# Kernel optimization log

Hardware: AMD Instinct MI355X
Metric: run time of the kernel (lower is better)

## Reference

```python
import jax, jax.numpy as jnp
import numpy as np

NUM_HEADS = 16
DIM = 1024
B, L = 2, 2048
NEG = -10000000000.0


def setup_inputs() -> dict:
    key = jax.random.key(0)
    ks = jax.random.split(key, 8)
    queries = jax.random.normal(ks[0], (B, L, DIM), dtype=jnp.float32)
    keys = jax.random.normal(ks[1], (B, L, DIM), dtype=jnp.float32)
    values = jax.random.normal(ks[2], (B, L, DIM), dtype=jnp.float32)
    mask = jax.random.uniform(ks[3], (B, L, L)) < 0.1
    s = 1.0 / np.sqrt(DIM)
    Wq = jax.random.uniform(ks[4], (DIM, DIM), minval=-s, maxval=s, dtype=jnp.float32)
    Wk = jax.random.uniform(ks[5], (DIM, DIM), minval=-s, maxval=s, dtype=jnp.float32)
    Wv = jax.random.uniform(ks[6], (DIM, DIM), minval=-s, maxval=s, dtype=jnp.float32)
    Wo = jax.random.uniform(ks[7], (DIM, DIM), minval=-s, maxval=s, dtype=jnp.float32)
    return {"queries": queries, "keys": keys, "values": values, "mask": mask,
            "Wq": Wq, "Wk": Wk, "Wv": Wv, "Wo": Wo}


def reference(queries, keys, values, mask, Wq, Wk, Wv, Wo):
    b, l, d = queries.shape
    h = NUM_HEADS
    dk = d // h
    # torch Linear(bias=False): y = x @ W.T ; then view(b, l, dk, h) -> head axis LAST
    qs = (queries @ Wq.T).reshape(b, l, dk, h)
    ks = (keys @ Wk.T).reshape(b, l, dk, h)
    vs = (values @ Wv.T).reshape(b, l, dk, h)
    # routing is None in the live code path
    w = jnp.einsum('bidh,bodh->bioh', qs, ks) / jnp.sqrt(jnp.asarray(dk, jnp.float32))
    w = jnp.where(mask[..., None], NEG, w)          # masked_fill where mask True
    w = jax.nn.softmax(w, axis=-2)                   # softmax over key axis 'o'
    mha = jnp.einsum('bioh,bodh->bidh', w, vs).reshape(b, l, d)
    # dropout is identity in eval mode
    return mha @ Wo.T
```

## Files before the change

kernel.cpp:

```cpp
#include <hip/hip_runtime.h>
#include <hip/hip_bf16.h>
#include <cstdint>
#include <cstddef>

typedef unsigned short ushort_t;
typedef __attribute__((ext_vector_type(8))) short short8;
typedef __attribute__((ext_vector_type(8))) unsigned short ushort8;
typedef __attribute__((ext_vector_type(4))) unsigned short ushort4v;
typedef __attribute__((ext_vector_type(4))) float f32x4;
typedef __attribute__((ext_vector_type(2))) unsigned long long ull2;

#define LPAD 72

__device__ __forceinline__ unsigned short f2bf(float f) {
    unsigned int x = __float_as_uint(f);
    unsigned int r = x + 0x7fffu + ((x >> 16) & 1u);
    return (unsigned short)(r >> 16);
}

__device__ __forceinline__ void async16(const ushort_t* g, ushort_t* l) {
    __builtin_amdgcn_global_load_lds(
        (const __attribute__((address_space(1))) unsigned int*)g,
        (__attribute__((address_space(3))) unsigned int*)l,
        16, 0, 0);
}

__global__ __launch_bounds__(256) void cvt(const float* __restrict__ q,
                                           const float* __restrict__ k,
                                           const float* __restrict__ v,
                                           const float* __restrict__ Wq,
                                           const float* __restrict__ Wk,
                                           const float* __restrict__ Wv,
                                           ushort_t* __restrict__ qb,
                                           ushort_t* __restrict__ kb,
                                           ushort_t* __restrict__ vb,
                                           ushort_t* __restrict__ Wqb,
                                           ushort_t* __restrict__ Wkb,
                                           ushort_t* __restrict__ Wvb) {
    const int z = blockIdx.y;
    const float* X = (z == 0) ? q : (z == 1) ? k : v;
    const float* W = (z == 0) ? Wq : (z == 1) ? Wk : Wv;
    ushort_t* Xo = (z == 0) ? qb : (z == 1) ? kb : vb;
    ushort_t* Wo2 = (z == 0) ? Wqb : (z == 1) ? Wkb : Wvb;
    const size_t idx = (((size_t)blockIdx.x << 8) + threadIdx.x) << 3;
    const float* src; ushort_t* dst; float sc = 1.0f;
    if (idx < 4194304) { src = X + idx; dst = Xo + idx; if (z == 0) sc = 0.125f; }
    else               { src = W + (idx - 4194304); dst = Wo2 + (idx - 4194304); }
    f32x4 a0 = *(const f32x4*)src, a1 = *(const f32x4*)(src + 4);
    ushort8 o;
    #pragma unroll
    for (int j = 0; j < 4; j++) { o[j] = f2bf(a0[j] * sc); o[j + 4] = f2bf(a1[j] * sc); }
    *(ushort8*)dst = o;
}

__global__ __launch_bounds__(256) void maskbits_kernel(const int* __restrict__ mask,
                                                       unsigned long long* __restrict__ Mbits) {
    const int row  = blockIdx.x;
    const int w    = threadIdx.x >> 6;
    const int lane = threadIdx.x & 63;
    const int* mrow = mask + (size_t)row * 2048;
    #pragma unroll
    for (int it = 0; it < 8; it++) {
        const int o = (it << 8) + (w << 6) + lane;
        const unsigned long long bb = __ballot(mrow[o] != 0);
        if (lane == 0) Mbits[(size_t)((it << 2) + w) * 4096 + row] = bb;
    }
}

__global__ __launch_bounds__(256) void woswz(const float* __restrict__ W,
                                             ushort_t* __restrict__ WoH) {
    __shared__ float row[1024 + 64];
    const int j = blockIdx.x, t = threadIdx.x;
    f32x4 v = *(const f32x4*)(W + (size_t)j * 1024 + (t << 2));
    #pragma unroll
    for (int s = 0; s < 4; s++) { const int c = (t << 2) + s; row[c + (c >> 4)] = v[s]; }
    __syncthreads();
    #pragma unroll
    for (int s = 0; s < 4; s++) {
        const int k = t + (s << 8);
        const int col = ((k & 63) << 4) + (k >> 6);
        WoH[(size_t)j * 1024 + k] = f2bf(row[col + (col >> 4)]);
    }
}

__global__ __launch_bounds__(256) void gemm_proj(const ushort_t* __restrict__ qb,
                                                 const ushort_t* __restrict__ kb,
                                                 const ushort_t* __restrict__ vb,
                                                 const ushort_t* __restrict__ Wqb,
                                                 const ushort_t* __restrict__ Wkb,
                                                 const ushort_t* __restrict__ Wvb,
                                                 ushort_t* __restrict__ Qh,
                                                 ushort_t* __restrict__ Kh,
                                                 ushort_t* __restrict__ VhT) {
    __shared__ ushort_t Xs[512 * 8];
    __shared__ ushort_t Ws[512 * 8];

    const int lid  = blockIdx.x;
    const int nIdx = lid / 96;
    const int rem  = lid % 96;
    const int z    = rem >> 5;
    const int mIdx = rem & 31;
    const int n0   = nIdx << 7;
    const int m0   = mIdx << 7;

    const ushort_t* Xb = (z == 0) ? qb : (z == 1) ? kb : vb;
    const ushort_t* Wb = (z == 0) ? Wqb : (z == 1) ? Wkb : Wvb;

    const int tid  = threadIdx.x;
    const int w    = tid >> 6;
    const int lane = tid & 63;
    const int lm   = lane & 15;
    const int quad = lane >> 4;
    const int wm   = w & 1;
    const int wn   = w >> 1;

    f32x4 acc[4][4];
    #pragma unroll
    for (int i = 0; i < 4; i++)
        #pragma unroll
        for (int j = 0; j < 4; j++) acc[i][j] = (f32x4){0.f, 0.f, 0.f, 0.f};

    for (int k0 = 0; k0 < 1024; k0 += 32) {
        __syncthreads();
        #pragma unroll
        for (int i = 0; i < 2; i++) {
            const int L   = (((w << 1) + i) << 6) + lane;
            const int c4  = L >> 7, row = L & 127;
            const int lb  = (((w << 1) + i) << 6) << 3;
            async16(Xb + (size_t)(m0 + row) * 1024 + k0 + (c4 << 3), &Xs[lb]);
            async16(Wb + (size_t)(n0 + row) * 1024 + k0 + (c4 << 3), &Ws[lb]);
        }
        __syncthreads();
        short8 af[4], bf4[4];
        #pragma unroll
        for (int mf = 0; mf < 4; mf++)
            af[mf] = *(const short8*)&Xs[((quad << 7) + (wm << 6) + (mf << 4) + lm) << 3];
        #pragma unroll
        for (int nf = 0; nf < 4; nf++)
            bf4[nf] = *(const short8*)&Ws[((quad << 7) + (wn << 6) + (nf << 4) + lm) << 3];
        #pragma unroll
        for (int mf = 0; mf < 4; mf++)
            #pragma unroll
            for (int nf = 0; nf < 4; nf++)
                acc[mf][nf] = __builtin_amdgcn_mfma_f32_16x16x32_bf16(af[mf], bf4[nf], acc[mf][nf], 0, 0, 0);
    }

    const int bb    = m0 >> 11;
    const int l0    = m0 & 2047;
    const int dbase = (n0 >> 4) + (wn << 2);
    if (z != 2) {
        ushort_t* OUT = (z == 0) ? Qh : Kh;
        #pragma unroll
        for (int mf = 0; mf < 4; mf++)
            #pragma unroll
            for (int r = 0; r < 4; r++) {
                const int row = (wm << 6) + (mf << 4) + (quad << 2) + r;
                ushort4v o = { f2bf(acc[mf][0][r]), f2bf(acc[mf][1][r]),
                               f2bf(acc[mf][2][r]), f2bf(acc[mf][3][r]) };
                *(ushort4v*)(OUT + ((size_t)((bb << 4) + lm) * 2048 + l0 + row) * 64 + dbase) = o;
            }
    } else {
        #pragma unroll
        for (int mf = 0; mf < 4; mf++)
            #pragma unroll
            for (int nf = 0; nf < 4; nf++) {
                const int lbase = l0 + (wm << 6) + (mf << 4) + (quad << 2);
                ushort4v o = { f2bf(acc[mf][nf][0]), f2bf(acc[mf][nf][1]),
                               f2bf(acc[mf][nf][2]), f2bf(acc[mf][nf][3]) };
                *(ushort4v*)(VhT + ((size_t)((bb << 4) + lm) * 64 + dbase + nf) * 2048 + lbase) = o;
            }
    }
}

__global__ __launch_bounds__(256) void gemm_out(const ushort_t* __restrict__ mhaH,
                                                const ushort_t* __restrict__ WoH,
                                                float* __restrict__ C) {
    __shared__ ushort_t Xs[256 * 8];
    __shared__ ushort_t Ws[256 * 8];
    const int tid  = threadIdx.x;
    const int m0   = blockIdx.y << 6;
    const int n0   = blockIdx.x << 6;
    const int w    = tid >> 6;
    const int lane = tid & 63;
    const int lm   = lane & 15;
    const int quad = lane >> 4;
    const int ab   = m0 >> 11;
    const int al0  = m0 & 2047;

    f32x4 acc[4] = {{0.f,0.f,0.f,0.f},{0.f,0.f,0.f,0.f},{0.f,0.f,0.f,0.f},{0.f,0.f,0.f,0.f}};

    for (int k0 = 0; k0 < 1024; k0 += 32) {
        const int h  = k0 >> 6;
        const int d0 = k0 & 63;
        __syncthreads();
        async16(mhaH + (((size_t)(ab * 16 + h)) * 2048 + al0 + lane) * 64 + d0 + (w << 3),
                &Xs[(w << 6) << 3]);
        async16(WoH + (size_t)(n0 + lane) * 1024 + k0 + (w << 3),
                &Ws[(w << 6) << 3]);
        __syncthreads();
        short8 af = *(const short8*)&Xs[((quad << 6) + (w << 4) + lm) << 3];
        #pragma unroll
        for (int c = 0; c < 4; c++) {
            short8 bf = *(const short8*)&Ws[((quad << 6) + (c << 4) + lm) << 3];
            acc[c] = __builtin_amdgcn_mfma_f32_16x16x32_bf16(af, bf, acc[c], 0, 0, 0);
        }
    }
    #pragma unroll
    for (int c = 0; c < 4; c++) {
        #pragma unroll
        for (int r = 0; r < 4; r++) {
            const int row = m0 + (w << 4) + (quad << 2) + r;
            const int col = n0 + (c << 4) + lm;
            C[(size_t)row * 1024 + col] = acc[c][r];
        }
    }
}

__global__ __launch_bounds__(256, 2) void flash_attn(const ushort_t* __restrict__ Qh,
                                                     const ushort_t* __restrict__ Kh,
                                                     const ushort_t* __restrict__ VhT,
                                                     const unsigned long long* __restrict__ Mbits,
                                                     ushort_t* __restrict__ mhaH) {
    __shared__ ushort_t Ks[64 * LPAD];
    __shared__ ushort_t Vt[64 * LPAD];
    __shared__ ushort_t Pw[4][16 * LPAD];

    const int tid  = threadIdx.x;
    const int w    = tid >> 6;
    const int lane = tid & 63;
    const int lm   = lane & 15;
    const int quad = lane >> 4;
    const int bh   = blockIdx.y;
    const int b    = bh >> 4;
    const int q0   = blockIdx.x << 7;

    const ushort_t* Qb  = Qh  + ((size_t)bh << 17);
    const ushort_t* Kb  = Kh  + ((size_t)bh << 17);
    const ushort_t* Vtb = VhT + ((size_t)bh << 17);

    short8 aq[2][2];
    #pragma unroll
    for (int g = 0; g < 2; g++) {
        const ushort_t* qp = Qb + (size_t)(q0 + (w << 5) + (g << 4) + lm) * 64 + (quad << 3);
        aq[g][0] = *(const short8*)qp;
        aq[g][1] = *(const short8*)(qp + 32);
    }

    float l_part[2][4] = {{0.f,0.f,0.f,0.f},{0.f,0.f,0.f,0.f}};
    f32x4 o_acc[2][4] = {{{0.f,0.f,0.f,0.f},{0.f,0.f,0.f,0.f},{0.f,0.f,0.f,0.f},{0.f,0.f,0.f,0.f}},
                         {{0.f,0.f,0.f,0.f},{0.f,0.f,0.f,0.f},{0.f,0.f,0.f,0.f},{0.f,0.f,0.f,0.f}}};

    const int chunk0  = tid << 1;
    const int rowbase = (b << 11) + q0 + (w << 5);

    for (int kt0 = 0; kt0 < 2048; kt0 += 64) {
        __syncthreads();
        #pragma unroll
        for (int cc = 0; cc < 2; cc++) {
            const int chunk = chunk0 + cc;
            const int rr = chunk >> 3;
            const int rc = (chunk & 7) << 3;
            *(ushort8*)&Ks[rr * LPAD + rc] =
                *(const ushort8*)(Kb + (size_t)(kt0 + rr) * 64 + rc);
            *(ushort8*)&Vt[rr * LPAD + rc] =
                *(const ushort8*)(Vtb + (size_t)rr * 2048 + kt0 + rc);
        }
        __syncthreads();

        short8 bk[4][2], bv[4][2];
        #pragma unroll
        for (int c = 0; c < 4; c++) {
            bk[c][0] = *(const short8*)&Ks[((c << 4) + lm) * LPAD + (quad << 3)];
            bk[c][1] = *(const short8*)&Ks[((c << 4) + lm) * LPAD + 32 + (quad << 3)];
            bv[c][0] = *(const short8*)&Vt[((c << 4) + lm) * LPAD + (quad << 3)];
            bv[c][1] = *(const short8*)&Vt[((c << 4) + lm) * LPAD + 32 + (quad << 3)];
        }

        const unsigned long long* Mt = Mbits + (size_t)(kt0 >> 6) * 4096 + rowbase;

        #pragma unroll
        for (int g = 0; g < 2; g++) {
            f32x4 s[4];
            #pragma unroll
            for (int c = 0; c < 4; c++) {
                f32x4 zz = {0.f, 0.f, 0.f, 0.f};
                zz = __builtin_amdgcn_mfma_f32_16x16x32_bf16(aq[g][0], bk[c][0], zz, 0, 0, 0);
                zz = __builtin_amdgcn_mfma_f32_16x16x32_bf16(aq[g][1], bk[c][1], zz, 0, 0, 0);
                s[c] = zz;
            }
            unsigned long long mb[4];
            {
                const unsigned long long* mp = Mt + (g << 4) + (quad << 2);
                ull2 t0 = *(const ull2*)mp;
                ull2 t1 = *(const ull2*)(mp + 2);
                mb[0] = t0[0]; mb[1] = t0[1]; mb[2] = t1[0]; mb[3] = t1[1];
            }
            #pragma unroll
            for (int r = 0; r < 4; r++) {
                const unsigned lo = (unsigned)mb[r];
                const unsigned hi = (unsigned)(mb[r] >> 32);
                float lsum = 0.f;
                #pragma unroll
                for (int c = 0; c < 4; c++) {
                    const unsigned word = (c & 2) ? hi : lo;
                    const unsigned bit = (word >> (((c & 1) << 4) + lm)) & 1u;
                    const float p = bit ? 0.f : __expf(s[c][r]);
                    s[c][r] = p;
                    lsum += p;
                }
                l_part[g][r] += lsum;
            }
            #pragma unroll
            for (int c = 0; c < 4; c++)
                #pragma unroll
                for (int r = 0; r < 4; r++)
                    Pw[w][((quad << 2) + r) * LPAD + (c << 4) + lm] = f2bf(s[c][r]);

            short8 ap0 = *(const short8*)&Pw[w][lm * LPAD + (quad << 3)];
            short8 ap1 = *(const short8*)&Pw[w][lm * LPAD + 32 + (quad << 3)];
            #pragma unroll
            for (int cd = 0; cd < 4; cd++) {
                o_acc[g][cd] = __builtin_amdgcn_mfma_f32_16x16x32_bf16(ap0, bv[cd][0], o_acc[g][cd], 0, 0, 0);
                o_acc[g][cd] = __builtin_amdgcn_mfma_f32_16x16x32_bf16(ap1, bv[cd][1], o_acc[g][cd], 0, 0, 0);
            }
        }
    }

    #pragma unroll
    for (int g = 0; g < 2; g++) {
        #pragma unroll
        for (int r = 0; r < 4; r++) {
            float l = l_part[g][r];
            l += __shfl_xor(l, 1, 64);
            l += __shfl_xor(l, 2, 64);
            l += __shfl_xor(l, 4, 64);
            l += __shfl_xor(l, 8, 64);
            const float inv_l = 1.0f / l;
            const int i = q0 + (w << 5) + (g << 4) + (quad << 2) + r;
            ushort_t* orow = mhaH + (((size_t)bh * 2048 + i) << 6);
            #pragma unroll
            for (int cd = 0; cd < 4; cd++)
                orow[(cd << 4) + lm] = f2bf(o_acc[g][cd][r] * inv_l);
        }
    }
}

extern "C" void kernel_launch(void* const* d_in, const int* in_sizes, int n_in,
                              void* d_out, int out_size, void* d_ws, size_t ws_size,
                              hipStream_t stream) {
    const float* q    = (const float*)d_in[0];
    const float* k    = (const float*)d_in[1];
    const float* v    = (const float*)d_in[2];
    const int*   mask = (const int*)d_in[3];
    const float* Wq   = (const float*)d_in[4];
    const float* Wk   = (const float*)d_in[5];
    const float* Wv   = (const float*)d_in[6];
    const float* Wo   = (const float*)d_in[7];
    float* out = (float*)d_out;

    ushort_t* qb   = (ushort_t*)d_ws;
    ushort_t* kb   = qb  + 4194304;
    ushort_t* vb   = kb  + 4194304;
    ushort_t* Wqb  = vb  + 4194304;
    ushort_t* Wkb  = Wqb + 1048576;
    ushort_t* Wvb  = Wkb + 1048576;
    ushort_t* Qh   = Wvb + 1048576;
    ushort_t* Kh   = Qh  + 4194304;
    ushort_t* VhT  = Kh  + 4194304;
    ushort_t* mhaH = qb;
    ushort_t* WoH  = kb;
    unsigned long long* Mbits = (unsigned long long*)(kb + 1048576);

    dim3 gb(256);
    cvt<<<dim3(2560, 3), gb, 0, stream>>>(q, k, v, Wq, Wk, Wv, qb, kb, vb, Wqb, Wkb, Wvb);
    gemm_proj<<<dim3(768), gb, 0, stream>>>(qb, kb, vb, Wqb, Wkb, Wvb, Qh, Kh, VhT);
    maskbits_kernel<<<dim3(4096), gb, 0, stream>>>(mask, Mbits);
    woswz<<<dim3(1024), gb, 0, stream>>>(Wo, WoH);
    flash_attn<<<dim3(16, 32), gb, 0, stream>>>(Qh, Kh, VhT, Mbits, mhaH);
    gemm_out<<<dim3(16, 64), gb, 0, stream>>>(mhaH, WoH, out);
}
```

Measured before the change: 326.9 us.

## Retile projection per head and load K/V fragments directly in attention

The projection GEMM now assigns each block one head (64 output columns gathered with stride 16) instead of 128 contiguous columns. This doubles the grid and changes the Q/K/V write pattern to per-head rows. The attention kernel drops its shared-memory K/V staging and the two barriers per tile, reading MFMA fragments straight from global memory. It also swaps the QK^T operand order so each lane owns one query row, which simplifies mask-bit extraction to one 64-bit load and lets the P tile be packed as 4-wide stores. The risks are uncoalesced, redundant global K/V reads across waves and a strided weight gather in the projection.

After: 379.1 us. 1.16x slower.

```diff
diff --git a/kernel.cpp b/kernel.cpp
--- a/kernel.cpp
+++ b/kernel.cpp
@@ -8,7 +8,6 @@
 typedef __attribute__((ext_vector_type(8))) unsigned short ushort8;
 typedef __attribute__((ext_vector_type(4))) unsigned short ushort4v;
 typedef __attribute__((ext_vector_type(4))) float f32x4;
-typedef __attribute__((ext_vector_type(2))) unsigned long long ull2;
 
 #define LPAD 72
 
@@ -93,14 +92,13 @@
                                                  ushort_t* __restrict__ Kh,
                                                  ushort_t* __restrict__ VhT) {
     __shared__ ushort_t Xs[512 * 8];
-    __shared__ ushort_t Ws[512 * 8];
+    __shared__ ushort_t Ws[256 * 8];
 
     const int lid  = blockIdx.x;
-    const int nIdx = lid / 96;
-    const int rem  = lid % 96;
-    const int z    = rem >> 5;
-    const int mIdx = rem & 31;
-    const int n0   = nIdx << 7;
+    const int z    = lid % 3;
+    const int rem  = lid / 3;
+    const int head = rem & 15;
+    const int mIdx = rem >> 4;
     const int m0   = mIdx << 7;
 
     const ushort_t* Xb = (z == 0) ? qb : (z == 1) ? kb : vb;
@@ -114,11 +112,11 @@
     const int wm   = w & 1;
     const int wn   = w >> 1;
 
-    f32x4 acc[4][4];
+    f32x4 acc[4][2];
     #pragma unroll
     for (int i = 0; i < 4; i++)
         #pragma unroll
-        for (int j = 0; j < 4; j++) acc[i][j] = (f32x4){0.f, 0.f, 0.f, 0.f};
+        for (int j = 0; j < 2; j++) acc[i][j] = (f32x4){0.f, 0.f, 0.f, 0.f};
 
     for (int k0 = 0; k0 < 1024; k0 += 32) {
         __syncthreads();
@@ -126,48 +124,54 @@
         for (int i = 0; i < 2; i++) {
             const int L   = (((w << 1) + i) << 6) + lane;
             const int c4  = L >> 7, row = L & 127;
-            const int lb  = (((w << 1) + i) << 6) << 3;
-            async16(Xb + (size_t)(m0 + row) * 1024 + k0 + (c4 << 3), &Xs[lb]);
-            async16(Wb + (size_t)(n0 + row) * 1024 + k0 + (c4 << 3), &Ws[lb]);
+            async16(Xb + (size_t)(m0 + row) * 1024 + k0 + (c4 << 3),
+                    &Xs[((((w << 1) + i) << 6) << 3)]);
+        }
+        {
+            const int j = head + (lane << 4);
+            async16(Wb + (size_t)j * 1024 + k0 + (w << 3), &Ws[((w << 6) << 3)]);
         }
         __syncthreads();
-        short8 af[4], bf4[4];
+        short8 af[4], bf2[2];
         #pragma unroll
         for (int mf = 0; mf < 4; mf++)
             af[mf] = *(const short8*)&Xs[((quad << 7) + (wm << 6) + (mf << 4) + lm) << 3];
         #pragma unroll
-        for (int nf = 0; nf < 4; nf++)
-            bf4[nf] = *(const short8*)&Ws[((quad << 7) + (wn << 6) + (nf << 4) + lm) << 3];
+        for (int nf = 0; nf < 2; nf++)
+            bf2[nf] = *(const short8*)&Ws[((quad << 6) + (wn << 5) + (nf << 4) + lm) << 3];
         #pragma unroll
         for (int mf = 0; mf < 4; mf++)
             #pragma unroll
-            for (int nf = 0; nf < 4; nf++)
-                acc[mf][nf] = __builtin_amdgcn_mfma_f32_16x16x32_bf16(af[mf], bf4[nf], acc[mf][nf], 0, 0, 0);
-    }
-
-    const int bb    = m0 >> 11;
-    const int l0    = m0 & 2047;
-    const int dbase = (n0 >> 4) + (wn << 2);
+            for (int nf = 0; nf < 2; nf++)
+                acc[mf][nf] = __builtin_amdgcn_mfma_f32_16x16x32_bf16(af[mf], bf2[nf], acc[mf][nf], 0, 0, 0);
+    }
+
+    const int bb = m0 >> 11;
+    const int l0 = m0 & 2047;
+    const size_t bh = (size_t)((bb << 4) + head);
     if (z != 2) {
         ushort_t* OUT = (z == 0) ? Qh : Kh;
         #pragma unroll
         for (int mf = 0; mf < 4; mf++)
             #pragma unroll
-            for (int r = 0; r < 4; r++) {
-                const int row = (wm << 6) + (mf << 4) + (quad << 2) + r;
-                ushort4v o = { f2bf(acc[mf][0][r]), f2bf(acc[mf][1][r]),
-                               f2bf(acc[mf][2][r]), f2bf(acc[mf][3][r]) };
-                *(ushort4v*)(OUT + ((size_t)((bb << 4) + lm) * 2048 + l0 + row) * 64 + dbase) = o;
+            for (int nf = 0; nf < 2; nf++) {
+                const int d = (wn << 5) + (nf << 4) + lm;
+                #pragma unroll
+                for (int r = 0; r < 4; r++) {
+                    const int l = l0 + (wm << 6) + (mf << 4) + (quad << 2) + r;
+                    OUT[((bh * 2048 + l) << 6) + d] = f2bf(acc[mf][nf][r]);
+                }
             }
     } else {
         #pragma unroll
         for (int mf = 0; mf < 4; mf++)
             #pragma unroll
-            for (int nf = 0; nf < 4; nf++) {
-                const int lbase = l0 + (wm << 6) + (mf << 4) + (quad << 2);
+            for (int nf = 0; nf < 2; nf++) {
+                const int d = (wn << 5) + (nf << 4) + lm;
+                const int l = l0 + (wm << 6) + (mf << 4) + (quad << 2);
                 ushort4v o = { f2bf(acc[mf][nf][0]), f2bf(acc[mf][nf][1]),
                                f2bf(acc[mf][nf][2]), f2bf(acc[mf][nf][3]) };
-                *(ushort4v*)(VhT + ((size_t)((bb << 4) + lm) * 64 + dbase + nf) * 2048 + lbase) = o;
+                *(ushort4v*)(VhT + ((bh << 6) + d) * 2048 + l) = o;
             }
     }
 }
@@ -221,8 +225,6 @@
                                                      const ushort_t* __restrict__ VhT,
                                                      const unsigned long long* __restrict__ Mbits,
                                                      ushort_t* __restrict__ mhaH) {
-    __shared__ ushort_t Ks[64 * LPAD];
-    __shared__ ushort_t Vt[64 * LPAD];
     __shared__ ushort_t Pw[4][16 * LPAD];
 
     const int tid  = threadIdx.x;
@@ -238,45 +240,32 @@
     const ushort_t* Kb  = Kh  + ((size_t)bh << 17);
     const ushort_t* Vtb = VhT + ((size_t)bh << 17);
 
-    short8 aq[2][2];
+    short8 bq[2][2];
     #pragma unroll
     for (int g = 0; g < 2; g++) {
         const ushort_t* qp = Qb + (size_t)(q0 + (w << 5) + (g << 4) + lm) * 64 + (quad << 3);
-        aq[g][0] = *(const short8*)qp;
-        aq[g][1] = *(const short8*)(qp + 32);
-    }
-
-    float l_part[2][4] = {{0.f,0.f,0.f,0.f},{0.f,0.f,0.f,0.f}};
+        bq[g][0] = *(const short8*)qp;
+        bq[g][1] = *(const short8*)(qp + 32);
+    }
+
+    float l_part[2] = {0.f, 0.f};
     f32x4 o_acc[2][4] = {{{0.f,0.f,0.f,0.f},{0.f,0.f,0.f,0.f},{0.f,0.f,0.f,0.f},{0.f,0.f,0.f,0.f}},
                          {{0.f,0.f,0.f,0.f},{0.f,0.f,0.f,0.f},{0.f,0.f,0.f,0.f},{0.f,0.f,0.f,0.f}}};
 
-    const int chunk0  = tid << 1;
-    const int rowbase = (b << 11) + q0 + (w << 5);
+    const int rowq = (b << 11) + q0 + (w << 5);
 
     for (int kt0 = 0; kt0 < 2048; kt0 += 64) {
-        __syncthreads();
-        #pragma unroll
-        for (int cc = 0; cc < 2; cc++) {
-            const int chunk = chunk0 + cc;
-            const int rr = chunk >> 3;
-            const int rc = (chunk & 7) << 3;
-            *(ushort8*)&Ks[rr * LPAD + rc] =
-                *(const ushort8*)(Kb + (size_t)(kt0 + rr) * 64 + rc);
-            *(ushort8*)&Vt[rr * LPAD + rc] =
-                *(const ushort8*)(Vtb + (size_t)rr * 2048 + kt0 + rc);
-        }
-        __syncthreads();
-
-        short8 bk[4][2], bv[4][2];
+        short8 ak[4][2], bv[4][2];
         #pragma unroll
         for (int c = 0; c < 4; c++) {
-            bk[c][0] = *(const short8*)&Ks[((c << 4) + lm) * LPAD + (quad << 3)];
-            bk[c][1] = *(const short8*)&Ks[((c << 4) + lm) * LPAD + 32 + (quad << 3)];
-            bv[c][0] = *(const short8*)&Vt[((c << 4) + lm) * LPAD + (quad << 3)];
-            bv[c][1] = *(const short8*)&Vt[((c << 4) + lm) * LPAD + 32 + (quad << 3)];
-        }
-
-        const unsigned long long* Mt = Mbits + (size_t)(kt0 >> 6) * 4096 + rowbase;
+            const ushort_t* kp = Kb + (size_t)(kt0 + (c << 4) + lm) * 64 + (quad << 3);
+            ak[c][0] = *(const short8*)kp;
+            ak[c][1] = *(const short8*)(kp + 32);
+            const ushort_t* vp = Vtb + (size_t)((c << 4) + lm) * 2048 + kt0 + (quad << 3);
+            bv[c][0] = *(const short8*)vp;
+            bv[c][1] = *(const short8*)(vp + 32);
+        }
+        const unsigned long long* Mt = Mbits + ((size_t)(kt0 >> 6) << 12) + rowq;
 
         #pragma unroll
         for (int g = 0; g < 2; g++) {
@@ -284,38 +273,28 @@
             #pragma unroll
             for (int c = 0; c < 4; c++) {
                 f32x4 zz = {0.f, 0.f, 0.f, 0.f};
-                zz = __builtin_amdgcn_mfma_f32_16x16x32_bf16(aq[g][0], bk[c][0], zz, 0, 0, 0);
-                zz = __builtin_amdgcn_mfma_f32_16x16x32_bf16(aq[g][1], bk[c][1], zz, 0, 0, 0);
+                zz = __builtin_amdgcn_mfma_f32_16x16x32_bf16(ak[c][0], bq[g][0], zz, 0, 0, 0);
+                zz = __builtin_amdgcn_mfma_f32_16x16x32_bf16(ak[c][1], bq[g][1], zz, 0, 0, 0);
                 s[c] = zz;
             }
-            unsigned long long mb[4];
-            {
-                const unsigned long long* mp = Mt + (g << 4) + (quad << 2);
-                ull2 t0 = *(const ull2*)mp;
-                ull2 t1 = *(const ull2*)(mp + 2);
-                mb[0] = t0[0]; mb[1] = t0[1]; mb[2] = t1[0]; mb[3] = t1[1];
-            }
-            #pragma unroll
-            for (int r = 0; r < 4; r++) {
-                const unsigned lo = (unsigned)mb[r];
-                const unsigned hi = (unsigned)(mb[r] >> 32);
-                float lsum = 0.f;
+            const unsigned long long M = Mt[(g << 4) + lm];
+            float lsum = 0.f;
+            #pragma unroll
+            for (int c = 0; c < 4; c++) {
                 #pragma unroll
-                for (int c = 0; c < 4; c++) {
-                    const unsigned word = (c & 2) ? hi : lo;
-                    const unsigned bit = (word >> (((c & 1) << 4) + lm)) & 1u;
+                for (int r = 0; r < 4; r++) {
+                    const unsigned bit = (unsigned)(M >> ((c << 4) + (quad << 2) + r)) & 1u;
                     const float p = bit ? 0.f : __expf(s[c][r]);
                     s[c][r] = p;
                     lsum += p;
                 }
-                l_part[g][r] += lsum;
-            }
-            #pragma unroll
-            for (int c = 0; c < 4; c++)
-                #pragma unroll
-                for (int r = 0; r < 4; r++)
-                    Pw[w][((quad << 2) + r) * LPAD + (c << 4) + lm] = f2bf(s[c][r]);
-
+            }
+            l_part[g] += lsum;
+            #pragma unroll
+            for (int c = 0; c < 4; c++) {
+                ushort4v pk = { f2bf(s[c][0]), f2bf(s[c][1]), f2bf(s[c][2]), f2bf(s[c][3]) };
+                *(ushort4v*)&Pw[w][lm * LPAD + (c << 4) + (quad << 2)] = pk;
+            }
             short8 ap0 = *(const short8*)&Pw[w][lm * LPAD + (quad << 3)];
             short8 ap1 = *(const short8*)&Pw[w][lm * LPAD + 32 + (quad << 3)];
             #pragma unroll
@@ -328,19 +307,18 @@
 
     #pragma unroll
     for (int g = 0; g < 2; g++) {
+        float l = l_part[g];
+        l += __shfl_xor(l, 16, 64);
+        l += __shfl_xor(l, 32, 64);
+        const float invl = 1.0f / l;
         #pragma unroll
         for (int r = 0; r < 4; r++) {
-            float l = l_part[g][r];
-            l += __shfl_xor(l, 1, 64);
-            l += __shfl_xor(l, 2, 64);
-            l += __shfl_xor(l, 4, 64);
-            l += __shfl_xor(l, 8, 64);
-            const float inv_l = 1.0f / l;
+            const float il = __shfl(invl, (quad << 2) + r, 64);
             const int i = q0 + (w << 5) + (g << 4) + (quad << 2) + r;
             ushort_t* orow = mhaH + (((size_t)bh * 2048 + i) << 6);
             #pragma unroll
             for (int cd = 0; cd < 4; cd++)
-                orow[(cd << 4) + lm] = f2bf(o_acc[g][cd][r] * inv_l);
+                orow[(cd << 4) + lm] = f2bf(o_acc[g][cd][r] * il);
         }
     }
 }
@@ -373,7 +351,7 @@
 
     dim3 gb(256);
     cvt<<<dim3(2560, 3), gb, 0, stream>>>(q, k, v, Wq, Wk, Wv, qb, kb, vb, Wqb, Wkb, Wvb);
-    gemm_proj<<<dim3(768), gb, 0, stream>>>(qb, kb, vb, Wqb, Wkb, Wvb, Qh, Kh, VhT);
+    gemm_proj<<<dim3(1536), gb, 0, stream>>>(qb, kb, vb, Wqb, Wkb, Wvb, Qh, Kh, VhT);
     maskbits_kernel<<<dim3(4096), gb, 0, stream>>>(mask, Mbits);
     woswz<<<dim3(1024), gb, 0, stream>>>(Wo, WoH);
     flash_attn<<<dim3(16, 32), gb, 0, stream>>>(Qh, Kh, VhT, Mbits, mhaH);
```
